# Optimization experiments

Measured on AMD Instinct MI355X. Metric: run time of the kernel, lower is better.

The kernel has to match this reference:

```python
import jax, jax.numpy as jnp
import numpy as np

N, L, BAG_NUM, NUM_CLASSES = 131072, 512, 512, 128
BIG_NEG = 65535.0  # matches torch code's (1-indicator)*65535 mask


def setup_inputs() -> dict:
    key = jax.random.key(0)
    k1, k2, k3, k4, k5 = jax.random.split(key, 5)
    H = jax.random.normal(k1, (N, L), dtype=jnp.float32)
    attention = jax.random.normal(k2, (1, N), dtype=jnp.float32)
    batch = jnp.sort(jax.random.randint(k3, (N,), 0, BAG_NUM)).astype(jnp.int64)
    fc1_w = jax.random.normal(k4, (NUM_CLASSES, L), dtype=jnp.float32) * 0.02
    fc1_b = jax.random.normal(k5, (NUM_CLASSES,), dtype=jnp.float32) * 0.02
    return {"H": H, "attention": attention, "batch": batch, "fc1_w": fc1_w, "fc1_b": fc1_b}


def reference(H, attention, batch, fc1_w, fc1_b):
    # pool_model='attention', paradigm='embedding'
    # indicator: (N, BAG_NUM) one-hot bag membership
    indicator = jax.nn.one_hot(batch, BAG_NUM, dtype=H.dtype)
    # A: broadcast per-instance attention score into its bag column
    A = attention.T * indicator                      # (N, BAG_NUM)
    # per-bag softmax over instances (dim 0), non-members pushed to -65535
    A = jax.nn.softmax(A - (1.0 - indicator) * BIG_NEG, axis=0)
    bag_feat = A.T @ H                               # (BAG_NUM, L)
    return bag_feat @ fc1_w.T + fc1_b                # (BAG_NUM, NUM_CLASSES)
```

## Files before the change

### kernel.cpp

```cpp
#include <hip/hip_runtime.h>
#include <math.h>

#define N_INST 131072
#define L_DIM 512
#define BAG_NUM 512
#define NUM_CLASSES 128
#define CHUNK 1024

__global__ void boundaries_kernel(const int* __restrict__ batch,
                                  int* __restrict__ start) {
    int i = blockIdx.x * blockDim.x + threadIdx.x;
    if (i >= N_INST) return;
    int b = batch[i];
    int prev = (i == 0) ? -1 : batch[i - 1];
    for (int bb = prev + 1; bb <= b; ++bb) start[bb] = i;
    if (i == N_INST - 1) {
        for (int bb = b + 1; bb <= BAG_NUM; ++bb) start[bb] = N_INST;
    }
}

__global__ __launch_bounds__(256) void bag_fused_kernel(
        const float* __restrict__ H, const float* __restrict__ att,
        const int* __restrict__ start, const float* __restrict__ fc1_w,
        const float* __restrict__ fc1_b, float* __restrict__ out) {
    int b = blockIdx.x;
    int tid = threadIdx.x;
    int c = tid & 127;
    int p = tid >> 7;

    int s = start[b], e = start[b + 1];

    __shared__ float red[8];
    __shared__ float wlds[CHUNK];
    __shared__ float4 cmb[128];
    __shared__ float fcred[256];

    float m = -3.4e38f;
    for (int i = s + tid; i < e; i += 256) m = fmaxf(m, att[i]);
    for (int off = 32; off >= 1; off >>= 1) m = fmaxf(m, __shfl_down(m, off));
    if ((tid & 63) == 0) red[tid >> 6] = m;
    __syncthreads();
    m = fmaxf(fmaxf(red[0], red[1]), fmaxf(red[2], red[3]));

    float sum = 0.f;
    for (int i = s + tid; i < e; i += 256) sum += expf(att[i] - m);
    for (int off = 32; off >= 1; off >>= 1) sum += __shfl_down(sum, off);
    if ((tid & 63) == 0) red[4 + (tid >> 6)] = sum;
    __syncthreads();
    float inv = 1.0f / (red[4] + red[5] + red[6] + red[7]);

    float4 acc = make_float4(0.f, 0.f, 0.f, 0.f);
    const float4* __restrict__ H4 = (const float4*)H;
    for (int c0 = s; c0 < e; c0 += CHUNK) {
        int ce = min(c0 + CHUNK, e);
        __syncthreads();
        for (int i = c0 + tid; i < ce; i += 256)
            wlds[i - c0] = expf(att[i] - m) * inv;
        __syncthreads();
        int i = c0;
        for (; i + 16 <= ce; i += 16) {
            float w[8];
            float4 h[8];
#pragma unroll
            for (int j = 0; j < 8; ++j) w[j] = wlds[i - c0 + p + 2 * j];
#pragma unroll
            for (int j = 0; j < 8; ++j)
                h[j] = H4[(size_t)(i + p + 2 * j) * 128 + c];
#pragma unroll
            for (int j = 0; j < 8; ++j) {
                acc.x = fmaf(w[j], h[j].x, acc.x);
                acc.y = fmaf(w[j], h[j].y, acc.y);
                acc.z = fmaf(w[j], h[j].z, acc.z);
                acc.w = fmaf(w[j], h[j].w, acc.w);
            }
        }
        for (; i + 2 <= ce; i += 2) {
            float w = wlds[i - c0 + p];
            float4 h = H4[(size_t)(i + p) * 128 + c];
            acc.x = fmaf(w, h.x, acc.x);
            acc.y = fmaf(w, h.y, acc.y);
            acc.z = fmaf(w, h.z, acc.z);
            acc.w = fmaf(w, h.w, acc.w);
        }
        if (i < ce && p == 0) {
            float w = wlds[i - c0];
            float4 h = H4[(size_t)i * 128 + c];
            acc.x = fmaf(w, h.x, acc.x);
            acc.y = fmaf(w, h.y, acc.y);
            acc.z = fmaf(w, h.z, acc.z);
            acc.w = fmaf(w, h.w, acc.w);
        }
    }

    if (p == 1) cmb[c] = acc;
    __syncthreads();
    if (p == 0) {
        float4 o = cmb[c];
        o.x += acc.x; o.y += acc.y; o.z += acc.z; o.w += acc.w;
        cmb[c] = o;
    }
    __syncthreads();

    {
        const float* rowf = (const float*)cmb;
        const float4* __restrict__ w4 =
            (const float4*)(fc1_w + (size_t)c * L_DIM + p * 256);
        const float4* __restrict__ r4 = (const float4*)(rowf + p * 256);
        float a = 0.f;
#pragma unroll 8
        for (int k4 = 0; k4 < 64; ++k4) {
            float4 wv = w4[k4];
            float4 rv = r4[k4];
            a = fmaf(wv.x, rv.x, a);
            a = fmaf(wv.y, rv.y, a);
            a = fmaf(wv.z, rv.z, a);
            a = fmaf(wv.w, rv.w, a);
        }
        fcred[tid] = a;
    }
    __syncthreads();
    if (tid < NUM_CLASSES)
        out[(size_t)b * NUM_CLASSES + tid] =
            fcred[tid] + fcred[tid + 128] + fc1_b[tid];
}

extern "C" void kernel_launch(void* const* d_in, const int* in_sizes, int n_in,
                              void* d_out, int out_size, void* d_ws, size_t ws_size,
                              hipStream_t stream) {
    const float* H     = (const float*)d_in[0];
    const float* att   = (const float*)d_in[1];
    const int*   batch = (const int*)d_in[2];
    const float* fc1_w = (const float*)d_in[3];
    const float* fc1_b = (const float*)d_in[4];
    float* out = (float*)d_out;

    int* start = (int*)d_ws;

    boundaries_kernel<<<N_INST / 256, 256, 0, stream>>>(batch, start);
    bag_fused_kernel<<<BAG_NUM, 256, 0, stream>>>(H, att, start, fc1_w, fc1_b, out);
}
```

Baseline: 383.2 us.

## Split bag accumulation across two column-half blocks and move FC to separate kernel

The fused per-bag kernel is split in two. The first launches two blocks per bag, each covering half of the 512 feature columns with four instance rows per iteration, and writes bag features to workspace. A second kernel then does the FC projection. This doubles the grid (1024 blocks over 256 CUs) for more parallelism and memory-level parallelism on the 268MB H stream. The cost is an extra launch, recomputing the softmax statistics in both blocks, and a round trip of the bag features through global memory.

New measurement: 386.3 us. Within noise of the previous version (+0.8%).

```diff
diff --git a/kernel.cpp b/kernel.cpp
--- a/kernel.cpp
+++ b/kernel.cpp
@@ -19,21 +19,20 @@
     }
 }
 
-__global__ __launch_bounds__(256) void bag_fused_kernel(
+__global__ __launch_bounds__(256) void bag_accum_kernel(
         const float* __restrict__ H, const float* __restrict__ att,
-        const int* __restrict__ start, const float* __restrict__ fc1_w,
-        const float* __restrict__ fc1_b, float* __restrict__ out) {
-    int b = blockIdx.x;
+        const int* __restrict__ start, float* __restrict__ bag_feat) {
+    int b = blockIdx.x >> 1;
+    int ch = blockIdx.x & 1;
     int tid = threadIdx.x;
-    int c = tid & 127;
-    int p = tid >> 7;
+    int r = tid >> 6;
+    int c4 = (tid & 63) + 64 * ch;
 
     int s = start[b], e = start[b + 1];
 
     __shared__ float red[8];
     __shared__ float wlds[CHUNK];
-    __shared__ float4 cmb[128];
-    __shared__ float fcred[256];
+    __shared__ float4 part[4][64];
 
     float m = -3.4e38f;
     for (int i = s + tid; i < e; i += 256) m = fmaxf(m, att[i]);
@@ -58,14 +57,14 @@
             wlds[i - c0] = expf(att[i] - m) * inv;
         __syncthreads();
         int i = c0;
-        for (; i + 16 <= ce; i += 16) {
+        for (; i + 32 <= ce; i += 32) {
             float w[8];
             float4 h[8];
 #pragma unroll
-            for (int j = 0; j < 8; ++j) w[j] = wlds[i - c0 + p + 2 * j];
+            for (int j = 0; j < 8; ++j) w[j] = wlds[i - c0 + r + 4 * j];
 #pragma unroll
             for (int j = 0; j < 8; ++j)
-                h[j] = H4[(size_t)(i + p + 2 * j) * 128 + c];
+                h[j] = H4[(size_t)(i + r + 4 * j) * 128 + c4];
 #pragma unroll
             for (int j = 0; j < 8; ++j) {
                 acc.x = fmaf(w[j], h[j].x, acc.x);
@@ -74,17 +73,17 @@
                 acc.w = fmaf(w[j], h[j].w, acc.w);
             }
         }
-        for (; i + 2 <= ce; i += 2) {
-            float w = wlds[i - c0 + p];
-            float4 h = H4[(size_t)(i + p) * 128 + c];
+        for (; i + 4 <= ce; i += 4) {
+            float w = wlds[i - c0 + r];
+            float4 h = H4[(size_t)(i + r) * 128 + c4];
             acc.x = fmaf(w, h.x, acc.x);
             acc.y = fmaf(w, h.y, acc.y);
             acc.z = fmaf(w, h.z, acc.z);
             acc.w = fmaf(w, h.w, acc.w);
         }
-        if (i < ce && p == 0) {
-            float w = wlds[i - c0];
-            float4 h = H4[(size_t)i * 128 + c];
+        if (i + r < ce) {
+            float w = wlds[i - c0 + r];
+            float4 h = H4[(size_t)(i + r) * 128 + c4];
             acc.x = fmaf(w, h.x, acc.x);
             acc.y = fmaf(w, h.y, acc.y);
             acc.z = fmaf(w, h.z, acc.z);
@@ -92,32 +91,49 @@
         }
     }
 
-    if (p == 1) cmb[c] = acc;
+    part[r][tid & 63] = acc;
     __syncthreads();
-    if (p == 0) {
-        float4 o = cmb[c];
-        o.x += acc.x; o.y += acc.y; o.z += acc.z; o.w += acc.w;
-        cmb[c] = o;
+    if (r == 0) {
+        int cl = tid & 63;
+        float4 a0 = part[0][cl], a1 = part[1][cl], a2 = part[2][cl], a3 = part[3][cl];
+        float4 o;
+        o.x = (a0.x + a1.x) + (a2.x + a3.x);
+        o.y = (a0.y + a1.y) + (a2.y + a3.y);
+        o.z = (a0.z + a1.z) + (a2.z + a3.z);
+        o.w = (a0.w + a1.w) + (a2.w + a3.w);
+        ((float4*)bag_feat)[(size_t)b * 128 + c4] = o;
     }
+}
+
+__global__ __launch_bounds__(256) void fc_kernel(
+        const float* __restrict__ bag_feat, const float* __restrict__ fc1_w,
+        const float* __restrict__ fc1_b, float* __restrict__ out) {
+    int b = blockIdx.x;
+    int tid = threadIdx.x;
+    int c = tid & 127;
+    int p = tid >> 7;
+
+    __shared__ float row[L_DIM];
+    __shared__ float fcred[256];
+
+    if (tid < 128)
+        ((float4*)row)[tid] = ((const float4*)(bag_feat + (size_t)b * L_DIM))[tid];
     __syncthreads();
 
-    {
-        const float* rowf = (const float*)cmb;
-        const float4* __restrict__ w4 =
-            (const float4*)(fc1_w + (size_t)c * L_DIM + p * 256);
-        const float4* __restrict__ r4 = (const float4*)(rowf + p * 256);
-        float a = 0.f;
+    const float4* __restrict__ w4 =
+        (const float4*)(fc1_w + (size_t)c * L_DIM + p * 256);
+    const float4* __restrict__ r4 = (const float4*)(row + p * 256);
+    float a = 0.f;
 #pragma unroll 8
-        for (int k4 = 0; k4 < 64; ++k4) {
-            float4 wv = w4[k4];
-            float4 rv = r4[k4];
-            a = fmaf(wv.x, rv.x, a);
-            a = fmaf(wv.y, rv.y, a);
-            a = fmaf(wv.z, rv.z, a);
-            a = fmaf(wv.w, rv.w, a);
-        }
-        fcred[tid] = a;
+    for (int k4 = 0; k4 < 64; ++k4) {
+        float4 wv = w4[k4];
+        float4 rv = r4[k4];
+        a = fmaf(wv.x, rv.x, a);
+        a = fmaf(wv.y, rv.y, a);
+        a = fmaf(wv.z, rv.z, a);
+        a = fmaf(wv.w, rv.w, a);
     }
+    fcred[tid] = a;
     __syncthreads();
     if (tid < NUM_CLASSES)
         out[(size_t)b * NUM_CLASSES + tid] =
@@ -134,8 +150,11 @@
     const float* fc1_b = (const float*)d_in[4];
     float* out = (float*)d_out;
 
-    int* start = (int*)d_ws;
+    char* ws = (char*)d_ws;
+    int*   start    = (int*)ws;
+    float* bag_feat = (float*)(ws + 4096);
 
     boundaries_kernel<<<N_INST / 256, 256, 0, stream>>>(batch, start);
-    bag_fused_kernel<<<BAG_NUM, 256, 0, stream>>>(H, att, start, fc1_w, fc1_b, out);
+    bag_accum_kernel<<<2 * BAG_NUM, 256, 0, stream>>>(H, att, start, bag_feat);
+    fc_kernel<<<BAG_NUM, 256, 0, stream>>>(bag_feat, fc1_w, fc1_b, out);
 }
```
